# Optimization experiments

Measured on AMD Instinct MI355X. Metric: run time of the kernel, lower is better.

The kernel has to match this reference:

```python
import jax, jax.numpy as jnp
import numpy as np
from jax import lax

IMG_H = IMG_W = 800.0
PRE_NMS = 2000      # rpn_pre_nms_top_n (test)
POST_NMS = 1000     # rpn_post_nms_top_n (test)
IOU_THR = 0.7       # rpn nms_thresh
MIN_SIZE = 1e-3     # filter_proposals min_size
SCORE_THR = 0.0     # rpn score_thresh
BBOX_CLIP = float(np.log(1000.0 / 16.0))  # torchvision BoxCoder bbox_xform_clip


def setup_inputs() -> dict:
    key = jax.random.key(0)
    k1, k2, k3, k4 = jax.random.split(key, 4)
    N, A = 8, 1_000_000
    objectness = jax.random.normal(k1, (N, A), jnp.float32)
    deltas = jax.random.normal(k2, (N, A, 4), jnp.float32) * 0.5
    # realistic anchors: random centers inside the image, sizes in [16, 256]
    cxy = jax.random.uniform(k3, (A, 2), jnp.float32) * jnp.array([IMG_W, IMG_H], jnp.float32)
    wh = 16.0 + jax.random.uniform(k4, (A, 2), jnp.float32) * 240.0
    anchors = jnp.concatenate([cxy - 0.5 * wh, cxy + 0.5 * wh], axis=-1)
    return {"objectness": objectness, "deltas": deltas, "anchors": anchors}


def decode_boxes(deltas, anchors):
    # torchvision BoxCoder.decode_single with weights (1,1,1,1)
    wa = anchors[:, 2] - anchors[:, 0]          # [A]
    ha = anchors[:, 3] - anchors[:, 1]
    cxa = anchors[:, 0] + 0.5 * wa
    cya = anchors[:, 1] + 0.5 * ha
    dx, dy = deltas[..., 0], deltas[..., 1]      # [N, A]
    dw = jnp.minimum(deltas[..., 2], BBOX_CLIP)
    dh = jnp.minimum(deltas[..., 3], BBOX_CLIP)
    pcx = dx * wa + cxa
    pcy = dy * ha + cya
    pw = jnp.exp(dw) * wa
    ph = jnp.exp(dh) * ha
    return jnp.stack([pcx - 0.5 * pw, pcy - 0.5 * ph,
                      pcx + 0.5 * pw, pcy + 0.5 * ph], axis=-1)  # [N, A, 4]


def nms_keep(boxes, valid):
    # greedy NMS on score-sorted boxes [K,4]; returns boolean keep mask [K]
    K = boxes.shape[0]
    areas = (boxes[:, 2] - boxes[:, 0]) * (boxes[:, 3] - boxes[:, 1])
    idxs = jnp.arange(K)

    def body(i, keep):
        xx1 = jnp.maximum(boxes[i, 0], boxes[:, 0])
        yy1 = jnp.maximum(boxes[i, 1], boxes[:, 1])
        xx2 = jnp.minimum(boxes[i, 2], boxes[:, 2])
        yy2 = jnp.minimum(boxes[i, 3], boxes[:, 3])
        inter = jnp.maximum(xx2 - xx1, 0.0) * jnp.maximum(yy2 - yy1, 0.0)
        iou = inter / (areas[i] + areas - inter + 1e-12)
        sup = (iou > IOU_THR) & (idxs > i) & keep[i]
        return keep & ~sup

    return lax.fori_loop(0, K, body, valid)


def filter_one(obj, boxes):
    # per-image filter_proposals: top-k -> sigmoid -> clip -> small-box removal -> NMS -> top post_nms
    top_logits, idx = lax.top_k(obj, PRE_NMS)        # sorted desc; sigmoid is monotone
    b = boxes[idx]                                    # [K, 4]
    scores = jax.nn.sigmoid(top_logits)
    x1 = jnp.clip(b[:, 0], 0.0, IMG_W)
    y1 = jnp.clip(b[:, 1], 0.0, IMG_H)
    x2 = jnp.clip(b[:, 2], 0.0, IMG_W)
    y2 = jnp.clip(b[:, 3], 0.0, IMG_H)
    bc = jnp.stack([x1, y1, x2, y2], axis=-1)
    valid = ((x2 - x1) >= MIN_SIZE) & ((y2 - y1) >= MIN_SIZE) & (scores > SCORE_THR)
    keep = nms_keep(lax.stop_gradient(bc), valid)     # selection is non-differentiable
    masked = jnp.where(keep, scores, -jnp.inf)
    _, fidx = lax.top_k(lax.stop_gradient(masked), POST_NMS)
    out_boxes = bc[fidx]                              # [POST_NMS, 4]
    out_scores = jnp.where(keep[fidx], scores[fidx], 0.0)
    return out_boxes, out_scores


def reference(objectness, deltas, anchors):
    proposals = decode_boxes(deltas, anchors)                 # [N, A, 4]
    boxes, scores = jax.vmap(filter_one)(objectness, proposals)
    return jnp.concatenate([boxes, scores[:, :, None]], axis=-1)  # [N, POST_NMS, 5]
```

## Files before the change

### kernel.cpp

```cpp
#include <hip/hip_runtime.h>
#include <cstdint>

#define NIMG 8
#define PRE 2000
#define POST 1000
#define NBINS 4096
#define CAND_CAP 8192
#define BLK_CAND_CAP 2048
#define PAIR_CAP 12288
#define BLK_PAIR_CAP 1024
#define JT 256
#define IMGW 800.0f
#define BBOX_CLIP_F 4.135166556742356f

#define OFF_HIST 0
#define OFF_INFO 131072
#define OFF_CCNT (OFF_INFO + 64)
#define OFF_PCNT (OFF_CCNT + 1024)
#define ZERO_BYTES 131072
#define OFF_CAND (OFF_PCNT + 1024)
#define OFF_BOX  (OFF_CAND + NIMG*CAND_CAP*8)
#define OFF_SCORE (OFF_BOX + NIMG*PRE*16)
#define OFF_VALID (OFF_SCORE + NIMG*PRE*4)
#define OFF_PAIRS (OFF_VALID + NIMG*PRE*4)

#define CNT_STRIDE 32

__device__ __forceinline__ unsigned int fkey(float f) {
    unsigned int b = __float_as_uint(f);
    return (b & 0x80000000u) ? ~b : (b | 0x80000000u);
}
__device__ __forceinline__ float inv_fkey(unsigned int k) {
    unsigned int b = (k & 0x80000000u) ? (k ^ 0x80000000u) : ~k;
    return __uint_as_float(b);
}

__global__ void k_zero(unsigned int* __restrict__ p, int n) {
    int i = blockIdx.x * blockDim.x + threadIdx.x;
    if (i < n) p[i] = 0u;
}

__global__ void k_hist(const float* __restrict__ obj, unsigned int* __restrict__ hist, int A) {
    __shared__ unsigned int h[NBINS];
    const int img = blockIdx.y;
    for (int i = threadIdx.x; i < NBINS; i += blockDim.x) h[i] = 0u;
    __syncthreads();
    const float4* p4 = (const float4*)(obj + (size_t)img * A);
    const int nvec = A >> 2;
    for (int i = blockIdx.x * blockDim.x + threadIdx.x; i < nvec; i += blockDim.x * gridDim.x) {
        float4 v = p4[i];
        atomicAdd(&h[fkey(v.x) >> 20], 1u);
        atomicAdd(&h[fkey(v.y) >> 20], 1u);
        atomicAdd(&h[fkey(v.z) >> 20], 1u);
        atomicAdd(&h[fkey(v.w) >> 20], 1u);
    }
    if (blockIdx.x == 0) {
        const float* p = obj + (size_t)img * A;
        for (int i = (nvec << 2) + threadIdx.x; i < A; i += blockDim.x)
            atomicAdd(&h[fkey(p[i]) >> 20], 1u);
    }
    __syncthreads();
    for (int i = threadIdx.x; i < NBINS; i += blockDim.x)
        if (h[i]) atomicAdd(&hist[img * NBINS + i], h[i]);
}

__global__ void k_scan(const unsigned int* __restrict__ hist, unsigned int* __restrict__ info,
                       unsigned int* __restrict__ ccnt, unsigned int* __restrict__ pcnt, int K) {
    __shared__ unsigned int seg[256];
    __shared__ unsigned int sufx[256];
    const int img = blockIdx.x;
    const int t = threadIdx.x;
    if (t == 0) { ccnt[img * CNT_STRIDE] = 0u; pcnt[img * CNT_STRIDE] = 0u; }
    const unsigned int* h = hist + img * NBINS;
    unsigned int loc[16];
    unsigned int s = 0;
#pragma unroll
    for (int k = 0; k < 16; ++k) { loc[k] = h[t * 16 + k]; s += loc[k]; }
    seg[t] = s;
    __syncthreads();
    if (t == 0) {
        unsigned int r = 0;
        for (int i = 255; i >= 0; --i) { sufx[i] = r; r += seg[i]; }
    }
    __syncthreads();
    unsigned int run = sufx[t];
#pragma unroll
    for (int k = 15; k >= 0; --k) {
        unsigned int nrun = run + loc[k];
        if (run < (unsigned int)K && nrun >= (unsigned int)K)
            info[img] = (unsigned int)(t * 16 + k);
        run = nrun;
    }
}

__global__ void k_compact(const float* __restrict__ obj, const unsigned int* __restrict__ info,
                          unsigned long long* __restrict__ cand, unsigned int* __restrict__ ccnt, int A) {
    __shared__ unsigned long long loc[BLK_CAND_CAP];
    __shared__ unsigned int lcnt, gbase;
    const int img = blockIdx.y;
    if (threadIdx.x == 0) lcnt = 0u;
    __syncthreads();
    const unsigned int kmin = info[img] << 20;
    const float4* p4 = (const float4*)(obj + (size_t)img * A);
    const int nvec = A >> 2;
    for (int i = blockIdx.x * blockDim.x + threadIdx.x; i < nvec; i += blockDim.x * gridDim.x) {
        float4 v = p4[i];
        unsigned int k0 = fkey(v.x), k1 = fkey(v.y), k2 = fkey(v.z), k3 = fkey(v.w);
        unsigned int base = (unsigned int)(i << 2);
        if (k0 >= kmin) { unsigned int p = atomicAdd(&lcnt, 1u); if (p < BLK_CAND_CAP) loc[p] = ((unsigned long long)k0 << 32) | (0xFFFFFFFFu - base); }
        if (k1 >= kmin) { unsigned int p = atomicAdd(&lcnt, 1u); if (p < BLK_CAND_CAP) loc[p] = ((unsigned long long)k1 << 32) | (0xFFFFFFFFu - (base + 1u)); }
        if (k2 >= kmin) { unsigned int p = atomicAdd(&lcnt, 1u); if (p < BLK_CAND_CAP) loc[p] = ((unsigned long long)k2 << 32) | (0xFFFFFFFFu - (base + 2u)); }
        if (k3 >= kmin) { unsigned int p = atomicAdd(&lcnt, 1u); if (p < BLK_CAND_CAP) loc[p] = ((unsigned long long)k3 << 32) | (0xFFFFFFFFu - (base + 3u)); }
    }
    if (blockIdx.x == 0) {
        const float* p = obj + (size_t)img * A;
        for (int i = (nvec << 2) + threadIdx.x; i < A; i += blockDim.x) {
            unsigned int k = fkey(p[i]);
            if (k >= kmin) { unsigned int pp = atomicAdd(&lcnt, 1u); if (pp < BLK_CAND_CAP) loc[pp] = ((unsigned long long)k << 32) | (0xFFFFFFFFu - (unsigned int)i); }
        }
    }
    __syncthreads();
    unsigned int n = min(lcnt, (unsigned int)BLK_CAND_CAP);
    if (threadIdx.x == 0 && n) gbase = atomicAdd(ccnt + img * CNT_STRIDE, n);
    __syncthreads();
    unsigned long long* c = cand + (size_t)img * CAND_CAP;
    for (unsigned int i = threadIdx.x; i < n; i += blockDim.x) {
        unsigned int p = gbase + i;
        if (p < CAND_CAP) c[p] = loc[i];
    }
}

__global__ __launch_bounds__(1024) void k_sort4(unsigned long long* __restrict__ cand,
                                                const unsigned int* __restrict__ ccnt) {
    __shared__ unsigned long long sb[2048];
    const int img = blockIdx.y;
    const int t = threadIdx.x;
    const int base = blockIdx.x * 2048;
    int n = (int)ccnt[img * CNT_STRIDE];
    if (n > CAND_CAP) n = CAND_CAP;
    unsigned long long* c = cand + (size_t)img * CAND_CAP;
    for (int i = t; i < 2048; i += 1024) {
        int g = base + i;
        sb[i] = (g < n) ? c[g] : 0ull;
    }
    __syncthreads();
    for (int k = 2; k <= 2048; k <<= 1) {
        for (int j = k >> 1; j > 0; j >>= 1) {
            for (int i = t; i < 2048; i += 1024) {
                int l = i ^ j;
                if (l > i) {
                    unsigned long long a = sb[i], b = sb[l];
                    bool sw = ((i & k) == 0) ? (a < b) : (a > b);
                    if (sw) { sb[i] = b; sb[l] = a; }
                }
            }
            __syncthreads();
        }
    }
    for (int i = t; i < 2048; i += 1024) c[base + i] = sb[i];
}

__global__ __launch_bounds__(1024) void k_merge_decode(
    const float* __restrict__ deltas, const float* __restrict__ anchors,
    const unsigned long long* __restrict__ cand,
    float* __restrict__ boxes, float* __restrict__ scores, unsigned int* __restrict__ valid, int A) {
    __shared__ unsigned long long sb[CAND_CAP];
    const int img = blockIdx.y;
    const int myseg = blockIdx.x;
    const int t = threadIdx.x;
    const unsigned long long* c = cand + (size_t)img * CAND_CAP;
    for (int i = t; i < CAND_CAP; i += 1024) sb[i] = c[i];
    __syncthreads();
    for (int e2 = t; e2 < 2048; e2 += 1024) {
        const int e = (myseg << 11) + e2;
        unsigned long long v = sb[e];
        if (v == 0ull) continue;
        int rank = e2;
#pragma unroll
        for (int s = 0; s < 4; ++s) {
            if (s == myseg) continue;
            int lo = 0, hi = 2048;
            const unsigned long long* seg = sb + (s << 11);
            while (lo < hi) {
                int mid = (lo + hi) >> 1;
                if (seg[mid] > v) lo = mid + 1; else hi = mid;
            }
            rank += lo;
        }
        if (rank >= PRE) continue;
        unsigned int idx = 0xFFFFFFFFu - (unsigned int)(v & 0xFFFFFFFFull);
        float logit = inv_fkey((unsigned int)(v >> 32));
        float4 d = ((const float4*)deltas)[(size_t)img * A + idx];
        float4 a = ((const float4*)anchors)[idx];
        float wa = a.z - a.x, ha = a.w - a.y;
        float cxa = a.x + 0.5f * wa, cya = a.y + 0.5f * ha;
        float dw = fminf(d.z, BBOX_CLIP_F), dh = fminf(d.w, BBOX_CLIP_F);
        float pcx = d.x * wa + cxa, pcy = d.y * ha + cya;
        float pw = expf(dw) * wa, ph = expf(dh) * ha;
        float x1 = fminf(fmaxf(pcx - 0.5f * pw, 0.0f), IMGW);
        float y1 = fminf(fmaxf(pcy - 0.5f * ph, 0.0f), IMGW);
        float x2 = fminf(fmaxf(pcx + 0.5f * pw, 0.0f), IMGW);
        float y2 = fminf(fmaxf(pcy + 0.5f * ph, 0.0f), IMGW);
        float sc = 1.0f / (1.0f + expf(-logit));
        unsigned int vd = (((x2 - x1) >= 1e-3f) && ((y2 - y1) >= 1e-3f) && (sc > 0.0f)) ? 1u : 0u;
        ((float4*)boxes)[(size_t)img * PRE + rank] = make_float4(x1, y1, x2, y2);
        scores[img * PRE + rank] = sc;
        valid[img * PRE + rank] = vd;
    }
}

__global__ void k_pairs(const float* __restrict__ boxes, unsigned int* __restrict__ pairs,
                        unsigned int* __restrict__ pcnt) {
#pragma clang fp contract(off)
    const int it = blockIdx.x >> 3;
    const int jc = blockIdx.x & 7;
    if (jc < it) return;
    __shared__ float4 jb[JT];
    __shared__ float jar[JT];
    __shared__ unsigned int lp[BLK_PAIR_CAP];
    __shared__ unsigned int lcnt, gbase;
    const int img = blockIdx.y;
    const int t = threadIdx.x;
    if (t == 0) lcnt = 0u;
    const float4* B = (const float4*)(boxes + (size_t)img * PRE * 4);
    const int j0 = jc * JT;
    const int jn = min(JT, PRE - j0);
    if (t < jn) {
        float4 b = B[j0 + t];
        jb[t] = b;
        jar[t] = (b.z - b.x) * (b.w - b.y);
    }
    const int i = it * JT + t;
    const bool alive = (i < PRE);
    float x1 = 0, y1 = 0, x2 = 0, y2 = 0, ai = 0;
    if (alive) {
        float4 b = B[i];
        x1 = b.x; y1 = b.y; x2 = b.z; y2 = b.w;
        ai = (b.z - b.x) * (b.w - b.y);
    }
    __syncthreads();
    if (alive) {
#pragma unroll 4
        for (int jj = 0; jj < jn; ++jj) {
            float4 bj = jb[jj];
            float aj = jar[jj];
            float xx1 = fmaxf(x1, bj.x);
            float yy1 = fmaxf(y1, bj.y);
            float xx2 = fminf(x2, bj.z);
            float yy2 = fminf(y2, bj.w);
            float iw = fmaxf(xx2 - xx1, 0.0f);
            float ih = fmaxf(yy2 - yy1, 0.0f);
            float inter = iw * ih;
            float iou = inter / (ai + aj - inter + 1e-12f);
            int j = j0 + jj;
            if (iou > 0.7f && j > i) {
                unsigned int p = atomicAdd(&lcnt, 1u);
                if (p < BLK_PAIR_CAP) lp[p] = ((unsigned int)i << 11) | (unsigned int)j;
            }
        }
    }
    __syncthreads();
    unsigned int n = min(lcnt, (unsigned int)BLK_PAIR_CAP);
    if (t == 0 && n) gbase = atomicAdd(pcnt + img * CNT_STRIDE, n);
    __syncthreads();
    unsigned int* pp = pairs + (size_t)img * PAIR_CAP;
    for (unsigned int q = t; q < n; q += blockDim.x) {
        unsigned int p = gbase + q;
        if (p < PAIR_CAP) pp[p] = lp[q];
    }
}

__global__ __launch_bounds__(1024) void k_final(
    const float* __restrict__ boxes, const float* __restrict__ scores, const unsigned int* __restrict__ valid,
    const unsigned int* __restrict__ pairs, const unsigned int* __restrict__ pcnt, float* __restrict__ out) {
    __shared__ unsigned int pb[PAIR_CAP];
    __shared__ unsigned char vld[2048];
    __shared__ unsigned char alive[2048];
    __shared__ unsigned char kill[2048];
    __shared__ unsigned int incl[2048];
    __shared__ int changed;
    const int img = blockIdx.x;
    const int t = threadIdx.x;
    int np = (int)pcnt[img * CNT_STRIDE];
    if (np > PAIR_CAP) np = PAIR_CAP;
    const unsigned int* ps = pairs + (size_t)img * PAIR_CAP;
    for (int i = t; i < np; i += 1024) pb[i] = ps[i];
    for (int i = t; i < 2048; i += 1024) {
        unsigned char v = (i < PRE) ? (unsigned char)valid[img * PRE + i] : 0;
        vld[i] = v;
        alive[i] = v;
    }
    __syncthreads();
    for (int iter = 0; iter < 2048; ++iter) {
        if (t == 0) changed = 0;
        for (int i = t; i < 2048; i += 1024) kill[i] = 0;
        __syncthreads();
        for (int e = t; e < np; e += 1024) {
            unsigned int u = pb[e];
            unsigned int i = u >> 11, j = u & 2047u;
            if (alive[i]) kill[j] = 1;
        }
        __syncthreads();
        for (int i = t; i < 2048; i += 1024) {
            unsigned char na = (vld[i] && !kill[i]) ? 1 : 0;
            if (na != alive[i]) { alive[i] = na; changed = 1; }
        }
        __syncthreads();
        bool done = (changed == 0);
        __syncthreads();
        if (done) break;
    }
    const int i0 = t, i1 = t + 1024;
    incl[i0] = alive[i0]; incl[i1] = alive[i1];
    __syncthreads();
    for (int d = 1; d < 2048; d <<= 1) {
        unsigned int v0 = (i0 >= d) ? incl[i0 - d] : 0u;
        unsigned int v1 = (i1 >= d) ? incl[i1 - d] : 0u;
        __syncthreads();
        incl[i0] += v0; incl[i1] += v1;
        __syncthreads();
    }
    const unsigned int Nk = incl[2047];
    for (int i = t; i < PRE; i += 1024) {
        int slot = -1;
        float sc = 0.0f;
        if (alive[i]) {
            unsigned int r = incl[i] - 1u;
            if (r < (unsigned int)POST) { slot = (int)r; sc = scores[img * PRE + i]; }
        } else if (Nk < (unsigned int)POST) {
            unsigned int rnk = (unsigned int)i - incl[i];
            unsigned int s2 = Nk + rnk;
            if (s2 < (unsigned int)POST) { slot = (int)s2; sc = 0.0f; }
        }
        if (slot >= 0) {
            float4 b = ((const float4*)boxes)[(size_t)img * PRE + i];
            float* o = out + ((size_t)img * POST + slot) * 5;
            o[0] = b.x; o[1] = b.y; o[2] = b.z; o[3] = b.w; o[4] = sc;
        }
    }
}

extern "C" void kernel_launch(void* const* d_in, const int* in_sizes, int n_in,
                              void* d_out, int out_size, void* d_ws, size_t ws_size,
                              hipStream_t stream) {
    const float* obj = (const float*)d_in[0];
    const float* deltas = (const float*)d_in[1];
    const float* anchors = (const float*)d_in[2];
    float* out = (float*)d_out;
    const int A = in_sizes[0] / NIMG;

    char* ws = (char*)d_ws;
    unsigned int* hist = (unsigned int*)(ws + OFF_HIST);
    unsigned int* info = (unsigned int*)(ws + OFF_INFO);
    unsigned int* ccnt = (unsigned int*)(ws + OFF_CCNT);
    unsigned int* pcnt = (unsigned int*)(ws + OFF_PCNT);
    unsigned long long* cand = (unsigned long long*)(ws + OFF_CAND);
    float* boxes = (float*)(ws + OFF_BOX);
    float* scores = (float*)(ws + OFF_SCORE);
    unsigned int* valid = (unsigned int*)(ws + OFF_VALID);
    unsigned int* pairs = (unsigned int*)(ws + OFF_PAIRS);

    const int nzero = ZERO_BYTES / 4;
    k_zero<<<dim3((nzero + 255) / 256), dim3(256), 0, stream>>>((unsigned int*)ws, nzero);
    k_hist<<<dim3(32, NIMG), dim3(256), 0, stream>>>(obj, hist, A);
    k_scan<<<dim3(NIMG), dim3(256), 0, stream>>>(hist, info, ccnt, pcnt, PRE);
    k_compact<<<dim3(64, NIMG), dim3(256), 0, stream>>>(obj, info, cand, ccnt, A);
    k_sort4<<<dim3(4, NIMG), dim3(1024), 0, stream>>>(cand, ccnt);
    k_merge_decode<<<dim3(4, NIMG), dim3(1024), 0, stream>>>(deltas, anchors, cand, boxes, scores, valid, A);
    k_pairs<<<dim3(64, NIMG), dim3(256), 0, stream>>>(boxes, pairs, pcnt);
    k_final<<<dim3(NIMG), dim3(1024), 0, stream>>>(boxes, scores, valid, pairs, pcnt, out);
}
```

Before: 303.9 us.

## Replace histogram top-k threshold with static key cutoff plus exact fallback

Drops the zero, histogram and scan kernels. Compaction now uses a fixed key threshold (logit 2.5) and writes into fixed per-chunk slots with per-chunk counts, so the objectness array is read only once and no global atomic counters are needed. A single-block fallback per image recomputes an exact histogram threshold if any chunk overflows or fewer than PRE candidates survive, so correctness does not depend on the input distribution. The pair-generation and final stages also move to per-block slots with prefix offsets instead of global atomics. The risk is that the fallback is a slow serial path whenever the static threshold does not fit the data.

Measured after the change: 300.4 us. About the same (-1.1%).

```diff
diff --git a/kernel.cpp b/kernel.cpp
--- a/kernel.cpp
+++ b/kernel.cpp
@@ -4,28 +4,29 @@
 #define NIMG 8
 #define PRE 2000
 #define POST 1000
-#define NBINS 4096
-#define CAND_CAP 8192
-#define BLK_CAND_CAP 2048
+#define NCH 64
+#define CH_CAP 256
+#define CAND_TOT (NCH*CH_CAP)
+#define NSORT 4
+#define SEG 2048
+#define CAND_MAX (NSORT*SEG)
+#define NPB 64
+#define PB_CAP 1024
 #define PAIR_CAP 12288
-#define BLK_PAIR_CAP 1024
 #define JT 256
 #define IMGW 800.0f
 #define BBOX_CLIP_F 4.135166556742356f
-
-#define OFF_HIST 0
-#define OFF_INFO 131072
-#define OFF_CCNT (OFF_INFO + 64)
-#define OFF_PCNT (OFF_CCNT + 1024)
-#define ZERO_BYTES 131072
-#define OFF_CAND (OFF_PCNT + 1024)
-#define OFF_BOX  (OFF_CAND + NIMG*CAND_CAP*8)
+#define STATIC_KMIN 0xC0200000u
+
+#define OFF_BCNT  0
+#define OFF_BPCNT (OFF_BCNT + NIMG*NCH*4)
+#define OFF_CAND  (OFF_BPCNT + NIMG*NPB*4)
+#define OFF_SRT   (OFF_CAND + NIMG*CAND_TOT*8)
+#define OFF_BOX   (OFF_SRT + NIMG*CAND_MAX*8)
 #define OFF_SCORE (OFF_BOX + NIMG*PRE*16)
 #define OFF_VALID (OFF_SCORE + NIMG*PRE*4)
 #define OFF_PAIRS (OFF_VALID + NIMG*PRE*4)
 
-#define CNT_STRIDE 32
-
 __device__ __forceinline__ unsigned int fkey(float f) {
     unsigned int b = __float_as_uint(f);
     return (b & 0x80000000u) ? ~b : (b | 0x80000000u);
@@ -35,118 +36,117 @@
     return __uint_as_float(b);
 }
 
-__global__ void k_zero(unsigned int* __restrict__ p, int n) {
-    int i = blockIdx.x * blockDim.x + threadIdx.x;
-    if (i < n) p[i] = 0u;
-}
-
-__global__ void k_hist(const float* __restrict__ obj, unsigned int* __restrict__ hist, int A) {
-    __shared__ unsigned int h[NBINS];
+__global__ void k_compact(const float* __restrict__ obj,
+                          unsigned long long* __restrict__ cand,
+                          unsigned int* __restrict__ bcnt, int A) {
+    __shared__ unsigned long long loc[CH_CAP];
+    __shared__ unsigned int lcnt;
     const int img = blockIdx.y;
-    for (int i = threadIdx.x; i < NBINS; i += blockDim.x) h[i] = 0u;
+    const int b = blockIdx.x;
+    const int t = threadIdx.x;
+    if (t == 0) lcnt = 0u;
     __syncthreads();
     const float4* p4 = (const float4*)(obj + (size_t)img * A);
     const int nvec = A >> 2;
-    for (int i = blockIdx.x * blockDim.x + threadIdx.x; i < nvec; i += blockDim.x * gridDim.x) {
-        float4 v = p4[i];
-        atomicAdd(&h[fkey(v.x) >> 20], 1u);
-        atomicAdd(&h[fkey(v.y) >> 20], 1u);
-        atomicAdd(&h[fkey(v.z) >> 20], 1u);
-        atomicAdd(&h[fkey(v.w) >> 20], 1u);
-    }
-    if (blockIdx.x == 0) {
-        const float* p = obj + (size_t)img * A;
-        for (int i = (nvec << 2) + threadIdx.x; i < A; i += blockDim.x)
-            atomicAdd(&h[fkey(p[i]) >> 20], 1u);
-    }
-    __syncthreads();
-    for (int i = threadIdx.x; i < NBINS; i += blockDim.x)
-        if (h[i]) atomicAdd(&hist[img * NBINS + i], h[i]);
-}
-
-__global__ void k_scan(const unsigned int* __restrict__ hist, unsigned int* __restrict__ info,
-                       unsigned int* __restrict__ ccnt, unsigned int* __restrict__ pcnt, int K) {
-    __shared__ unsigned int seg[256];
-    __shared__ unsigned int sufx[256];
-    const int img = blockIdx.x;
-    const int t = threadIdx.x;
-    if (t == 0) { ccnt[img * CNT_STRIDE] = 0u; pcnt[img * CNT_STRIDE] = 0u; }
-    const unsigned int* h = hist + img * NBINS;
-    unsigned int loc[16];
-    unsigned int s = 0;
-#pragma unroll
-    for (int k = 0; k < 16; ++k) { loc[k] = h[t * 16 + k]; s += loc[k]; }
-    seg[t] = s;
-    __syncthreads();
-    if (t == 0) {
-        unsigned int r = 0;
-        for (int i = 255; i >= 0; --i) { sufx[i] = r; r += seg[i]; }
-    }
-    __syncthreads();
-    unsigned int run = sufx[t];
-#pragma unroll
-    for (int k = 15; k >= 0; --k) {
-        unsigned int nrun = run + loc[k];
-        if (run < (unsigned int)K && nrun >= (unsigned int)K)
-            info[img] = (unsigned int)(t * 16 + k);
-        run = nrun;
-    }
-}
-
-__global__ void k_compact(const float* __restrict__ obj, const unsigned int* __restrict__ info,
-                          unsigned long long* __restrict__ cand, unsigned int* __restrict__ ccnt, int A) {
-    __shared__ unsigned long long loc[BLK_CAND_CAP];
-    __shared__ unsigned int lcnt, gbase;
-    const int img = blockIdx.y;
-    if (threadIdx.x == 0) lcnt = 0u;
-    __syncthreads();
-    const unsigned int kmin = info[img] << 20;
-    const float4* p4 = (const float4*)(obj + (size_t)img * A);
-    const int nvec = A >> 2;
-    for (int i = blockIdx.x * blockDim.x + threadIdx.x; i < nvec; i += blockDim.x * gridDim.x) {
+    for (int i = b * 256 + t; i < nvec; i += NCH * 256) {
         float4 v = p4[i];
         unsigned int k0 = fkey(v.x), k1 = fkey(v.y), k2 = fkey(v.z), k3 = fkey(v.w);
         unsigned int base = (unsigned int)(i << 2);
-        if (k0 >= kmin) { unsigned int p = atomicAdd(&lcnt, 1u); if (p < BLK_CAND_CAP) loc[p] = ((unsigned long long)k0 << 32) | (0xFFFFFFFFu - base); }
-        if (k1 >= kmin) { unsigned int p = atomicAdd(&lcnt, 1u); if (p < BLK_CAND_CAP) loc[p] = ((unsigned long long)k1 << 32) | (0xFFFFFFFFu - (base + 1u)); }
-        if (k2 >= kmin) { unsigned int p = atomicAdd(&lcnt, 1u); if (p < BLK_CAND_CAP) loc[p] = ((unsigned long long)k2 << 32) | (0xFFFFFFFFu - (base + 2u)); }
-        if (k3 >= kmin) { unsigned int p = atomicAdd(&lcnt, 1u); if (p < BLK_CAND_CAP) loc[p] = ((unsigned long long)k3 << 32) | (0xFFFFFFFFu - (base + 3u)); }
-    }
-    if (blockIdx.x == 0) {
+        if (k0 >= STATIC_KMIN) { unsigned int p = atomicAdd(&lcnt, 1u); if (p < CH_CAP) loc[p] = ((unsigned long long)k0 << 32) | (0xFFFFFFFFu - base); }
+        if (k1 >= STATIC_KMIN) { unsigned int p = atomicAdd(&lcnt, 1u); if (p < CH_CAP) loc[p] = ((unsigned long long)k1 << 32) | (0xFFFFFFFFu - (base + 1u)); }
+        if (k2 >= STATIC_KMIN) { unsigned int p = atomicAdd(&lcnt, 1u); if (p < CH_CAP) loc[p] = ((unsigned long long)k2 << 32) | (0xFFFFFFFFu - (base + 2u)); }
+        if (k3 >= STATIC_KMIN) { unsigned int p = atomicAdd(&lcnt, 1u); if (p < CH_CAP) loc[p] = ((unsigned long long)k3 << 32) | (0xFFFFFFFFu - (base + 3u)); }
+    }
+    if (b == 0) {
         const float* p = obj + (size_t)img * A;
-        for (int i = (nvec << 2) + threadIdx.x; i < A; i += blockDim.x) {
+        for (int i = (nvec << 2) + t; i < A; i += 256) {
             unsigned int k = fkey(p[i]);
-            if (k >= kmin) { unsigned int pp = atomicAdd(&lcnt, 1u); if (pp < BLK_CAND_CAP) loc[pp] = ((unsigned long long)k << 32) | (0xFFFFFFFFu - (unsigned int)i); }
-        }
-    }
-    __syncthreads();
-    unsigned int n = min(lcnt, (unsigned int)BLK_CAND_CAP);
-    if (threadIdx.x == 0 && n) gbase = atomicAdd(ccnt + img * CNT_STRIDE, n);
-    __syncthreads();
-    unsigned long long* c = cand + (size_t)img * CAND_CAP;
-    for (unsigned int i = threadIdx.x; i < n; i += blockDim.x) {
-        unsigned int p = gbase + i;
-        if (p < CAND_CAP) c[p] = loc[i];
-    }
-}
-
-__global__ __launch_bounds__(1024) void k_sort4(unsigned long long* __restrict__ cand,
-                                                const unsigned int* __restrict__ ccnt) {
-    __shared__ unsigned long long sb[2048];
+            if (k >= STATIC_KMIN) { unsigned int q = atomicAdd(&lcnt, 1u); if (q < CH_CAP) loc[q] = ((unsigned long long)k << 32) | (0xFFFFFFFFu - (unsigned int)i); }
+        }
+    }
+    __syncthreads();
+    if (t == 0) bcnt[img * NCH + b] = lcnt;
+    unsigned int n = min(lcnt, (unsigned int)CH_CAP);
+    unsigned long long* dst = cand + (size_t)img * CAND_TOT + (size_t)b * CH_CAP;
+    for (unsigned int i = t; i < n; i += 256) dst[i] = loc[i];
+}
+
+__global__ __launch_bounds__(1024) void k_fallback(const float* __restrict__ obj,
+                                                   unsigned long long* __restrict__ cand,
+                                                   unsigned int* __restrict__ bcnt, int A) {
+    __shared__ unsigned int h[4096];
+    __shared__ unsigned int cnts[NCH];
+    __shared__ int need_s;
+    __shared__ unsigned int kth_s, c2;
+    const int img = blockIdx.x;
+    const int t = threadIdx.x;
+    if (t < NCH) cnts[t] = bcnt[img * NCH + t];
+    __syncthreads();
+    if (t == 0) {
+        unsigned int tot = 0; int bad = 0;
+        for (int c = 0; c < NCH; ++c) { unsigned int r = cnts[c]; if (r > CH_CAP) bad = 1; tot += min(r, (unsigned int)CH_CAP); }
+        for (int g = 0; g < NSORT; ++g) {
+            unsigned int s = 0;
+            for (int c = 0; c < NCH / NSORT; ++c) s += min(cnts[g * (NCH / NSORT) + c], (unsigned int)CH_CAP);
+            if (s > SEG) bad = 1;
+        }
+        if (tot < PRE) bad = 1;
+        need_s = bad;
+    }
+    __syncthreads();
+    if (!need_s) return;
+    for (int i = t; i < 4096; i += 1024) h[i] = 0u;
+    __syncthreads();
+    const float* p = obj + (size_t)img * A;
+    for (int i = t; i < A; i += 1024) atomicAdd(&h[fkey(p[i]) >> 20], 1u);
+    __syncthreads();
+    if (t == 0) {
+        unsigned int run = 0, kb = 0;
+        for (int b = 4095; b >= 0; --b) { run += h[b]; if (run >= (unsigned int)PRE) { kb = (unsigned int)b; break; } }
+        kth_s = kb << 20; c2 = 0u;
+    }
+    __syncthreads();
+    for (int i = t; i < A; i += 1024) {
+        unsigned int k = fkey(p[i]);
+        if (k >= kth_s) {
+            unsigned int q = atomicAdd(&c2, 1u);
+            if (q < CAND_MAX)
+                cand[(size_t)img * CAND_TOT + (size_t)(q & (NCH - 1)) * CH_CAP + (q >> 6)] =
+                    ((unsigned long long)k << 32) | (0xFFFFFFFFu - (unsigned int)i);
+        }
+    }
+    __syncthreads();
+    unsigned int tot = min(c2, (unsigned int)CAND_MAX);
+    if (t < NCH) bcnt[img * NCH + t] = (tot + (NCH - 1) - t) >> 6;
+}
+
+__global__ __launch_bounds__(1024) void k_sort(const unsigned long long* __restrict__ cand,
+                                               const unsigned int* __restrict__ bcnt,
+                                               unsigned long long* __restrict__ srt) {
+    __shared__ unsigned long long sb[SEG];
+    __shared__ unsigned int pref[17];
     const int img = blockIdx.y;
-    const int t = threadIdx.x;
-    const int base = blockIdx.x * 2048;
-    int n = (int)ccnt[img * CNT_STRIDE];
-    if (n > CAND_CAP) n = CAND_CAP;
-    unsigned long long* c = cand + (size_t)img * CAND_CAP;
-    for (int i = t; i < 2048; i += 1024) {
-        int g = base + i;
-        sb[i] = (g < n) ? c[g] : 0ull;
-    }
-    __syncthreads();
-    for (int k = 2; k <= 2048; k <<= 1) {
+    const int s = blockIdx.x;
+    const int t = threadIdx.x;
+    if (t == 0) {
+        unsigned int o = 0; pref[0] = 0;
+        for (int c = 0; c < 16; ++c) {
+            unsigned int n = min(bcnt[img * NCH + s * 16 + c], (unsigned int)CH_CAP);
+            o += n; if (o > (unsigned int)SEG) o = SEG;
+            pref[c + 1] = o;
+        }
+    }
+    for (int i = t; i < SEG; i += 1024) sb[i] = 0ull;
+    __syncthreads();
+    for (int c = 0; c < 16; ++c) {
+        unsigned int b0 = pref[c], n = pref[c + 1] - pref[c];
+        const unsigned long long* src = cand + (size_t)img * CAND_TOT + (size_t)(s * 16 + c) * CH_CAP;
+        for (unsigned int i = t; i < n; i += 1024) sb[b0 + i] = src[i];
+    }
+    __syncthreads();
+    for (int k = 2; k <= SEG; k <<= 1) {
         for (int j = k >> 1; j > 0; j >>= 1) {
-            for (int i = t; i < 2048; i += 1024) {
+            for (int i = t; i < SEG; i += 1024) {
                 int l = i ^ j;
                 if (l > i) {
                     unsigned long long a = sb[i], b = sb[l];
@@ -157,21 +157,22 @@
             __syncthreads();
         }
     }
-    for (int i = t; i < 2048; i += 1024) c[base + i] = sb[i];
+    unsigned long long* dst = srt + (size_t)img * CAND_MAX + (size_t)s * SEG;
+    for (int i = t; i < SEG; i += 1024) dst[i] = sb[i];
 }
 
 __global__ __launch_bounds__(1024) void k_merge_decode(
     const float* __restrict__ deltas, const float* __restrict__ anchors,
-    const unsigned long long* __restrict__ cand,
+    const unsigned long long* __restrict__ srt,
     float* __restrict__ boxes, float* __restrict__ scores, unsigned int* __restrict__ valid, int A) {
-    __shared__ unsigned long long sb[CAND_CAP];
+    __shared__ unsigned long long sb[CAND_MAX];
     const int img = blockIdx.y;
     const int myseg = blockIdx.x;
     const int t = threadIdx.x;
-    const unsigned long long* c = cand + (size_t)img * CAND_CAP;
-    for (int i = t; i < CAND_CAP; i += 1024) sb[i] = c[i];
-    __syncthreads();
-    for (int e2 = t; e2 < 2048; e2 += 1024) {
+    const unsigned long long* c = srt + (size_t)img * CAND_MAX;
+    for (int i = t; i < CAND_MAX; i += 1024) sb[i] = c[i];
+    __syncthreads();
+    for (int e2 = t; e2 < SEG; e2 += 1024) {
         const int e = (myseg << 11) + e2;
         unsigned long long v = sb[e];
         if (v == 0ull) continue;
@@ -179,7 +180,7 @@
 #pragma unroll
         for (int s = 0; s < 4; ++s) {
             if (s == myseg) continue;
-            int lo = 0, hi = 2048;
+            int lo = 0, hi = SEG;
             const unsigned long long* seg = sb + (s << 11);
             while (lo < hi) {
                 int mid = (lo + hi) >> 1;
@@ -210,17 +211,18 @@
 }
 
 __global__ void k_pairs(const float* __restrict__ boxes, unsigned int* __restrict__ pairs,
-                        unsigned int* __restrict__ pcnt) {
+                        unsigned int* __restrict__ bpcnt) {
 #pragma clang fp contract(off)
-    const int it = blockIdx.x >> 3;
-    const int jc = blockIdx.x & 7;
-    if (jc < it) return;
+    const int img = blockIdx.y;
+    const int bid = blockIdx.x;
+    const int it = bid >> 3;
+    const int jc = bid & 7;
+    const int t = threadIdx.x;
+    if (jc < it) { if (t == 0) bpcnt[img * NPB + bid] = 0u; return; }
     __shared__ float4 jb[JT];
     __shared__ float jar[JT];
-    __shared__ unsigned int lp[BLK_PAIR_CAP];
-    __shared__ unsigned int lcnt, gbase;
-    const int img = blockIdx.y;
-    const int t = threadIdx.x;
+    __shared__ unsigned int lp[PB_CAP];
+    __shared__ unsigned int lcnt;
     if (t == 0) lcnt = 0u;
     const float4* B = (const float4*)(boxes + (size_t)img * PRE * 4);
     const int j0 = jc * JT;
@@ -231,15 +233,15 @@
         jar[t] = (b.z - b.x) * (b.w - b.y);
     }
     const int i = it * JT + t;
-    const bool alive = (i < PRE);
+    const bool row_ok = (i < PRE);
     float x1 = 0, y1 = 0, x2 = 0, y2 = 0, ai = 0;
-    if (alive) {
+    if (row_ok) {
         float4 b = B[i];
         x1 = b.x; y1 = b.y; x2 = b.z; y2 = b.w;
         ai = (b.z - b.x) * (b.w - b.y);
     }
     __syncthreads();
-    if (alive) {
+    if (row_ok) {
 #pragma unroll 4
         for (int jj = 0; jj < jn; ++jj) {
             float4 bj = jb[jj];
@@ -255,25 +257,23 @@
             int j = j0 + jj;
             if (iou > 0.7f && j > i) {
                 unsigned int p = atomicAdd(&lcnt, 1u);
-                if (p < BLK_PAIR_CAP) lp[p] = ((unsigned int)i << 11) | (unsigned int)j;
+                if (p < PB_CAP) lp[p] = ((unsigned int)i << 11) | (unsigned int)j;
             }
         }
     }
     __syncthreads();
-    unsigned int n = min(lcnt, (unsigned int)BLK_PAIR_CAP);
-    if (t == 0 && n) gbase = atomicAdd(pcnt + img * CNT_STRIDE, n);
-    __syncthreads();
-    unsigned int* pp = pairs + (size_t)img * PAIR_CAP;
-    for (unsigned int q = t; q < n; q += blockDim.x) {
-        unsigned int p = gbase + q;
-        if (p < PAIR_CAP) pp[p] = lp[q];
-    }
+    unsigned int n = min(lcnt, (unsigned int)PB_CAP);
+    if (t == 0) bpcnt[img * NPB + bid] = n;
+    unsigned int* dst = pairs + ((size_t)img * NPB + bid) * PB_CAP;
+    for (unsigned int q = t; q < n; q += blockDim.x) dst[q] = lp[q];
 }
 
 __global__ __launch_bounds__(1024) void k_final(
     const float* __restrict__ boxes, const float* __restrict__ scores, const unsigned int* __restrict__ valid,
-    const unsigned int* __restrict__ pairs, const unsigned int* __restrict__ pcnt, float* __restrict__ out) {
+    const unsigned int* __restrict__ pairs, const unsigned int* __restrict__ bpcnt, float* __restrict__ out) {
     __shared__ unsigned int pb[PAIR_CAP];
+    __shared__ unsigned int bp[NPB];
+    __shared__ unsigned int ofs[NPB + 1];
     __shared__ unsigned char vld[2048];
     __shared__ unsigned char alive[2048];
     __shared__ unsigned char kill[2048];
@@ -281,15 +281,24 @@
     __shared__ int changed;
     const int img = blockIdx.x;
     const int t = threadIdx.x;
-    int np = (int)pcnt[img * CNT_STRIDE];
-    if (np > PAIR_CAP) np = PAIR_CAP;
-    const unsigned int* ps = pairs + (size_t)img * PAIR_CAP;
-    for (int i = t; i < np; i += 1024) pb[i] = ps[i];
+    if (t < NPB) bp[t] = min(bpcnt[img * NPB + t], (unsigned int)PB_CAP);
+    __syncthreads();
+    if (t == 0) {
+        unsigned int o = 0; ofs[0] = 0;
+        for (int c = 0; c < NPB; ++c) { o += bp[c]; if (o > (unsigned int)PAIR_CAP) o = PAIR_CAP; ofs[c + 1] = o; }
+    }
     for (int i = t; i < 2048; i += 1024) {
         unsigned char v = (i < PRE) ? (unsigned char)valid[img * PRE + i] : 0;
         vld[i] = v;
         alive[i] = v;
     }
+    __syncthreads();
+    for (int c = 0; c < NPB; ++c) {
+        unsigned int b0 = ofs[c], n = ofs[c + 1] - ofs[c];
+        const unsigned int* src = pairs + ((size_t)img * NPB + c) * PB_CAP;
+        for (unsigned int i = t; i < n; i += 1024) pb[b0 + i] = src[i];
+    }
+    const int np = (int)ofs[NPB];
     __syncthreads();
     for (int iter = 0; iter < 2048; ++iter) {
         if (t == 0) changed = 0;
@@ -350,23 +359,19 @@
     const int A = in_sizes[0] / NIMG;
 
     char* ws = (char*)d_ws;
-    unsigned int* hist = (unsigned int*)(ws + OFF_HIST);
-    unsigned int* info = (unsigned int*)(ws + OFF_INFO);
-    unsigned int* ccnt = (unsigned int*)(ws + OFF_CCNT);
-    unsigned int* pcnt = (unsigned int*)(ws + OFF_PCNT);
+    unsigned int* bcnt = (unsigned int*)(ws + OFF_BCNT);
+    unsigned int* bpcnt = (unsigned int*)(ws + OFF_BPCNT);
     unsigned long long* cand = (unsigned long long*)(ws + OFF_CAND);
+    unsigned long long* srt = (unsigned long long*)(ws + OFF_SRT);
     float* boxes = (float*)(ws + OFF_BOX);
     float* scores = (float*)(ws + OFF_SCORE);
     unsigned int* valid = (unsigned int*)(ws + OFF_VALID);
     unsigned int* pairs = (unsigned int*)(ws + OFF_PAIRS);
 
-    const int nzero = ZERO_BYTES / 4;
-    k_zero<<<dim3((nzero + 255) / 256), dim3(256), 0, stream>>>((unsigned int*)ws, nzero);
-    k_hist<<<dim3(32, NIMG), dim3(256), 0, stream>>>(obj, hist, A);
-    k_scan<<<dim3(NIMG), dim3(256), 0, stream>>>(hist, info, ccnt, pcnt, PRE);
-    k_compact<<<dim3(64, NIMG), dim3(256), 0, stream>>>(obj, info, cand, ccnt, A);
-    k_sort4<<<dim3(4, NIMG), dim3(1024), 0, stream>>>(cand, ccnt);
-    k_merge_decode<<<dim3(4, NIMG), dim3(1024), 0, stream>>>(deltas, anchors, cand, boxes, scores, valid, A);
-    k_pairs<<<dim3(64, NIMG), dim3(256), 0, stream>>>(boxes, pairs, pcnt);
-    k_final<<<dim3(NIMG), dim3(1024), 0, stream>>>(boxes, scores, valid, pairs, pcnt, out);
-}
+    k_compact<<<dim3(NCH, NIMG), dim3(256), 0, stream>>>(obj, cand, bcnt, A);
+    k_fallback<<<dim3(NIMG), dim3(1024), 0, stream>>>(obj, cand, bcnt, A);
+    k_sort<<<dim3(NSORT, NIMG), dim3(1024), 0, stream>>>(cand, bcnt, srt);
+    k_merge_decode<<<dim3(NSORT, NIMG), dim3(1024), 0, stream>>>(deltas, anchors, srt, boxes, scores, valid, A);
+    k_pairs<<<dim3(NPB, NIMG), dim3(256), 0, stream>>>(boxes, pairs, bpcnt);
+    k_final<<<dim3(NIMG), dim3(1024), 0, stream>>>(boxes, scores, valid, pairs, bpcnt, out);
+}
```
